# Performance work log

Hardware: AMD Instinct MI355X
Metric: run time of the kernel (lower is better)

Reference implementation:

```python
import jax, jax.numpy as jnp
import numpy as np

B, DM, NH, NL, NP = 4, 768, 12, 3, 4
HD = DM // NH
H_IMG, W_IMG = 896, 896
LEVELS = [(H_IMG // 8, W_IMG // 8), (H_IMG // 16, W_IMG // 16), (H_IMG // 32, W_IMG // 32)]
QH, QW = H_IMG // 14, W_IMG // 14
LQ = QH * QW            # 4096 query tokens (stride-14 ViT grid)
LIN = sum(h * w for h, w in LEVELS)  # 16464 multi-scale value tokens


def setup_inputs() -> dict:
    key = jax.random.key(0)
    ks = jax.random.split(key, 14)
    s = 0.02
    return {
        "query": jax.random.normal(ks[0], (B, LQ, DM), jnp.float32),
        "feat": jax.random.normal(ks[1], (B, LIN, DM), jnp.float32),
        "ln_q_g": jnp.ones((DM,), jnp.float32),
        "ln_q_b": jnp.zeros((DM,), jnp.float32),
        "ln_f_g": jnp.ones((DM,), jnp.float32),
        "ln_f_b": jnp.zeros((DM,), jnp.float32),
        "W_off": jax.random.normal(ks[2], (DM, NH * NL * NP * 2), jnp.float32) * s,
        "b_off": jax.random.normal(ks[3], (NH * NL * NP * 2,), jnp.float32) * s,
        "W_attn": jax.random.normal(ks[4], (DM, NH * NL * NP), jnp.float32) * s,
        "b_attn": jax.random.normal(ks[5], (NH * NL * NP,), jnp.float32) * s,
        "W_val": jax.random.normal(ks[6], (DM, DM), jnp.float32) * s,
        "b_val": jnp.zeros((DM,), jnp.float32),
        "W_out": jax.random.normal(ks[7], (DM, DM), jnp.float32) * s,
        "b_out": jnp.zeros((DM,), jnp.float32),
        "gamma": jax.random.normal(ks[8], (DM,), jnp.float32) * s,
    }


def _ln(x, g, b, eps=1e-6):
    m = x.mean(-1, keepdims=True)
    v = ((x - m) ** 2).mean(-1, keepdims=True)
    return (x - m) * jax.lax.rsqrt(v + eps) * g + b


def _ref_points():
    # get_reference_points for the stride-14 query grid; pixel-center coords normalized
    ry, rx = jnp.meshgrid(
        (jnp.arange(QH, dtype=jnp.float32) + 0.5) / QH,
        (jnp.arange(QW, dtype=jnp.float32) + 0.5) / QW,
        indexing="ij",
    )
    return jnp.stack([rx.reshape(-1), ry.reshape(-1)], -1)  # (LQ, 2) in (x, y)


def _sample_level(v, loc, h_, w_):
    # v: (B, h_, w_, NH, HD); loc: (B, LQ, NH, NP, 2) normalized [0,1]
    # torch grid_sample bilinear, align_corners=False, zero padding
    x = loc[..., 0] * w_ - 0.5
    y = loc[..., 1] * h_ - 0.5
    x0 = jnp.floor(x)
    y0 = jnp.floor(y)
    wx = (x - x0)[..., None]
    wy = (y - y0)[..., None]
    x0i = x0.astype(jnp.int32)
    y0i = y0.astype(jnp.int32)
    bi = jnp.arange(B)[:, None, None, None]
    hi = jnp.arange(NH)[None, None, :, None]

    def g(yi, xi):
        valid = ((xi >= 0) & (xi < w_) & (yi >= 0) & (yi < h_)).astype(v.dtype)
        got = v[bi, jnp.clip(yi, 0, h_ - 1), jnp.clip(xi, 0, w_ - 1), hi]  # (B,LQ,NH,NP,HD)
        return got * valid[..., None]

    v00 = g(y0i, x0i)
    v01 = g(y0i, x0i + 1)
    v10 = g(y0i + 1, x0i)
    v11 = g(y0i + 1, x0i + 1)
    return v00 * (1 - wx) * (1 - wy) + v01 * wx * (1 - wy) + v10 * (1 - wx) * wy + v11 * wx * wy


def _injector(query, feat, ln_q_g, ln_q_b, ln_f_g, ln_f_b, W_off, b_off, W_attn, b_attn,
              W_val, b_val, W_out, b_out, gamma):
    q = _ln(query, ln_q_g, ln_q_b)
    f = _ln(feat, ln_f_g, ln_f_b)
    value = (f @ W_val + b_val).reshape(B, LIN, NH, HD)
    off = (q @ W_off + b_off).reshape(B, LQ, NH, NL, NP, 2)
    aw = jax.nn.softmax((q @ W_attn + b_attn).reshape(B, LQ, NH, NL * NP), axis=-1)
    aw = aw.reshape(B, LQ, NH, NL, NP)
    ref = _ref_points()  # (LQ, 2)
    offset_norm = jnp.array([[w, h] for h, w in LEVELS], jnp.float32)  # (NL, 2) = (W_, H_)
    loc = ref[None, :, None, None, None, :] + off / offset_norm[None, None, None, :, None, :]
    outs = []
    start = 0
    for lvl, (h_, w_) in enumerate(LEVELS):
        v = value[:, start:start + h_ * w_].reshape(B, h_, w_, NH, HD)
        outs.append(_sample_level(v, loc[:, :, :, lvl], h_, w_))
        start += h_ * w_
    samp = jnp.stack(outs, axis=3)  # (B, LQ, NH, NL, NP, HD)
    attn_out = (samp * aw[..., None]).sum(axis=(3, 4)).reshape(B, LQ, DM)
    attn_out = attn_out @ W_out + b_out
    return query + gamma * attn_out


def reference(query, feat, ln_q_g, ln_q_b, ln_f_g, ln_f_b, W_off, b_off, W_attn, b_attn,
              W_val, b_val, W_out, b_out, gamma):
    return _injector(query, feat, ln_q_g, ln_q_b, ln_f_g, ln_f_b, W_off, b_off, W_attn,
                     b_attn, W_val, b_val, W_out, b_out, gamma)
```

## Files before the change

### kernel.cpp

```cpp
#include <hip/hip_runtime.h>
#include <hip/hip_bf16.h>

typedef __hip_bfloat16 bf16;

#define BB    4
#define LQ    4096
#define LIN   16464
#define DM    768
#define NH    12
#define HD    64
#define K_DIM 768

typedef __attribute__((ext_vector_type(8))) __bf16 bfrag;
typedef __attribute__((ext_vector_type(4))) float  ffrag;

__device__ __forceinline__ void g2l16(const void* g, void* l) {
    __builtin_amdgcn_global_load_lds(
        (const __attribute__((address_space(1))) void*)g,
        (__attribute__((address_space(3))) void*)l, 16, 0, 0);
}

__device__ __forceinline__ int xcd_swz(int orig, int nwg) {
    int xcd = orig & 7, within = orig >> 3;
    int q = nwg >> 3, r = nwg & 7;
    return (xcd < r ? xcd * (q + 1) : r * (q + 1) + (xcd - r) * q) + within;
}

__global__ __launch_bounds__(256) void ln_kernel(
    const float* __restrict__ x, const float* __restrict__ g,
    const float* __restrict__ beta, bf16* __restrict__ y)
{
    int r = blockIdx.x * 4 + (threadIdx.x >> 6);
    int lane = threadIdx.x & 63;
    const float4* xr = (const float4*)(x + (size_t)r * DM);
    float4 v[3];
    #pragma unroll
    for (int i = 0; i < 3; i++) v[i] = xr[lane + 64 * i];
    float s = 0.f, ss = 0.f;
    #pragma unroll
    for (int i = 0; i < 3; i++) {
        s  += v[i].x + v[i].y + v[i].z + v[i].w;
        ss += v[i].x * v[i].x + v[i].y * v[i].y + v[i].z * v[i].z + v[i].w * v[i].w;
    }
    #pragma unroll
    for (int m = 1; m <= 32; m <<= 1) {
        s  += __shfl_xor(s, m);
        ss += __shfl_xor(ss, m);
    }
    float mean = s * (1.f / DM);
    float inv  = rsqrtf(ss * (1.f / DM) - mean * mean + 1e-6f);
    bf16* yr = y + (size_t)r * DM;
    #pragma unroll
    for (int i = 0; i < 3; i++) {
        float4 gg = ((const float4*)g)[lane + 64 * i];
        float4 bb = ((const float4*)beta)[lane + 64 * i];
        union { bf16 h[4]; uint2 u; } p;
        p.h[0] = __float2bfloat16((v[i].x - mean) * inv * gg.x + bb.x);
        p.h[1] = __float2bfloat16((v[i].y - mean) * inv * gg.y + bb.y);
        p.h[2] = __float2bfloat16((v[i].z - mean) * inv * gg.z + bb.z);
        p.h[3] = __float2bfloat16((v[i].w - mean) * inv * gg.w + bb.w);
        *(uint2*)(yr + (lane + 64 * i) * 4) = p.u;
    }
}

__global__ __launch_bounds__(256) void cast_transpose(
    const float* __restrict__ W, bf16* __restrict__ Wt, int N)
{
    __shared__ float t[32][33];
    int n0 = blockIdx.x * 32, k0 = blockIdx.y * 32;
    int tx = threadIdx.x & 31, ty = threadIdx.x >> 5;
    #pragma unroll
    for (int i = 0; i < 4; i++) {
        int k = k0 + ty + i * 8;
        int n = n0 + tx;
        t[ty + i * 8][tx] = (n < N) ? W[(size_t)k * N + n] : 0.f;
    }
    __syncthreads();
    #pragma unroll
    for (int i = 0; i < 4; i++) {
        int n = n0 + ty + i * 8;
        Wt[(size_t)n * K_DIM + k0 + tx] = __float2bfloat16(t[tx][ty + i * 8]);
    }
}

__global__ __launch_bounds__(512) void gemm256_value(
    const bf16*  __restrict__ A,
    const bf16*  __restrict__ Bt,
    const float* __restrict__ bias,
    bf16*        __restrict__ C,
    int M, int N)
{
    __shared__ __align__(16) char lds[98304];

    int tid  = threadIdx.x;
    int lane = tid & 63;
    int wave = tid >> 6;

    int nwg  = gridDim.x * gridDim.y;
    int orig = blockIdx.y * gridDim.x + blockIdx.x;
    int wg   = xcd_swz(orig, nwg);
    int bn = (wg % gridDim.x) * 256;
    int bm = (wg / gridDim.x) * 256;

    int ahalf = wave >> 2;
    int wc    = (wave & 3) * 64;

    int mrow = lane & 15;
    int kqs  = (((lane >> 4) ^ ((mrow >> 1) & 3)) * 8);

    ffrag acc[8][4] = {};

    int rA = tid >> 2;
    int kb = (((tid & 3) ^ ((rA >> 1) & 3)) * 8);
    int ra0 = min(bm + rA, M - 1), ra1 = min(bm + 128 + rA, M - 1);
    const bf16* gA0 = A  + (size_t)ra0 * K_DIM + kb;
    const bf16* gA1 = A  + (size_t)ra1 * K_DIM + kb;
    const bf16* gB0 = Bt + (size_t)(bn + rA) * K_DIM + kb;
    const bf16* gB1 = Bt + (size_t)(bn + 128 + rA) * K_DIM + kb;

    auto stage = [&](char* buf, int kt) {
        const int ko = kt * 32;
        g2l16(gA0 + ko, buf + tid * 16);
        g2l16(gA1 + ko, buf + tid * 16 + 8192);
        g2l16(gB0 + ko, buf + 16384 + tid * 16);
        g2l16(gB1 + ko, buf + 16384 + tid * 16 + 8192);
    };

    char* b0 = lds;
    char* b1 = lds + 32768;
    char* b2 = lds + 65536;
    stage(b0, 0); stage(b1, 1); stage(b2, 2);

    #pragma unroll
    for (int kt = 0; kt < 24; kt++) {
        if (kt + 2 < 24)      asm volatile("s_waitcnt vmcnt(8)" ::: "memory");
        else if (kt + 1 < 24) asm volatile("s_waitcnt vmcnt(4)" ::: "memory");
        else                  asm volatile("s_waitcnt vmcnt(0)" ::: "memory");
        __builtin_amdgcn_s_barrier();

        const char* Ab = b0 + (ahalf * 128) * 64;
        const char* Bb = b0 + 16384 + wc * 64;
        bfrag af[8], bf[4];
        #pragma unroll
        for (int mr = 0; mr < 8; mr++)
            af[mr] = *(const bfrag*)(Ab + (mr * 16 + mrow) * 64 + kqs * 2);
        #pragma unroll
        for (int nc = 0; nc < 4; nc++)
            bf[nc] = *(const bfrag*)(Bb + (nc * 16 + mrow) * 64 + kqs * 2);

        __builtin_amdgcn_s_setprio(1);
        #pragma unroll
        for (int mr = 0; mr < 8; mr++)
            #pragma unroll
            for (int nc = 0; nc < 4; nc++)
                acc[mr][nc] = __builtin_amdgcn_mfma_f32_16x16x32_bf16(
                    af[mr], bf[nc], acc[mr][nc], 0, 0, 0);
        __builtin_amdgcn_s_setprio(0);

        __builtin_amdgcn_s_barrier();
        if (kt + 3 < 24) stage(b0, kt + 3);
        char* tp = b0; b0 = b1; b1 = b2; b2 = tp;
    }

    int q4 = (lane >> 4) * 4;
    #pragma unroll
    for (int mr = 0; mr < 8; mr++) {
        #pragma unroll
        for (int rr = 0; rr < 4; rr++) {
            int rg = bm + ahalf * 128 + mr * 16 + q4 + rr;
            if (rg < M) {
                #pragma unroll
                for (int nc = 0; nc < 4; nc++) {
                    int cg = bn + wc + nc * 16 + mrow;
                    C[(size_t)rg * N + cg] =
                        __float2bfloat16(acc[mr][nc][rr] + bias[cg]);
                }
            }
        }
    }
}

__device__ __forceinline__ void gemm128_body(
    const bf16*  __restrict__ A,
    const bf16*  __restrict__ Bt,
    const float* __restrict__ bias,
    void*        __restrict__ C,
    const float* __restrict__ resid,
    const float* __restrict__ gamma,
    const float* __restrict__ bias2,
    int M, int N, int mode, int nsplit, char* lds)
{
    int tid  = threadIdx.x;
    int lane = tid & 63;

    int nwg  = gridDim.x * gridDim.y;
    int orig = blockIdx.y * gridDim.x + blockIdx.x;
    int wg = xcd_swz(orig, nwg);
    int bn = (wg % gridDim.x) * 128;
    int bm = (wg / gridDim.x) * 128;

    int wave = tid >> 6;
    int wr = (wave & 1) * 64, wc = (wave >> 1) * 64;

    ffrag acc[4][4] = {};

    int rA = tid >> 2;
    int kb = (((tid & 3) ^ ((rA >> 1) & 3)) * 8);
    int ra0 = min(bm + rA, M - 1), ra1 = min(bm + 64 + rA, M - 1);
    const bf16* gA0 = A  + (size_t)ra0 * K_DIM + kb;
    const bf16* gA1 = A  + (size_t)ra1 * K_DIM + kb;
    const bf16* gB0 = Bt + (size_t)(bn + rA) * K_DIM + kb;
    const bf16* gB1 = Bt + (size_t)(bn + 64 + rA) * K_DIM + kb;

    int mrow = lane & 15;
    int kqs  = (((lane >> 4) ^ ((mrow >> 1) & 3)) * 8);

    auto stage = [&](char* buf, int kt) {
        const int ko = kt * 32;
        g2l16(gA0 + ko, buf + tid * 16);
        g2l16(gA1 + ko, buf + tid * 16 + 4096);
        g2l16(gB0 + ko, buf + 8192 + tid * 16);
        g2l16(gB1 + ko, buf + 8192 + tid * 16 + 4096);
    };

    stage(lds, 0);
    asm volatile("s_waitcnt vmcnt(0)" ::: "memory");
    __builtin_amdgcn_s_barrier();

    #pragma unroll
    for (int kt = 0; kt < 24; kt++) {
        char* cur = lds + (kt & 1) * 16384;
        char* nxt = lds + ((kt & 1) ^ 1) * 16384;
        if (kt + 1 < 24) stage(nxt, kt + 1);

        bfrag a[4], b[4];
        #pragma unroll
        for (int t = 0; t < 4; t++) {
            a[t] = *(const bfrag*)(cur + ((wr + t * 16 + mrow) * 32 + kqs) * 2);
            b[t] = *(const bfrag*)(cur + 8192 + ((wc + t * 16 + mrow) * 32 + kqs) * 2);
        }
        __builtin_amdgcn_s_setprio(1);
        #pragma unroll
        for (int i = 0; i < 4; i++)
            #pragma unroll
            for (int j = 0; j < 4; j++)
                acc[i][j] = __builtin_amdgcn_mfma_f32_16x16x32_bf16(
                    a[i], b[j], acc[i][j], 0, 0, 0);
        __builtin_amdgcn_s_setprio(0);

        asm volatile("s_waitcnt vmcnt(0)" ::: "memory");
        __builtin_amdgcn_s_barrier();
    }

    int q4 = (lane >> 4) * 4;
    #pragma unroll
    for (int i = 0; i < 4; i++) {
        #pragma unroll
        for (int rr = 0; rr < 4; rr++) {
            int rg = bm + wr + i * 16 + q4 + rr;
            if (rg < M) {
                #pragma unroll
                for (int j = 0; j < 4; j++) {
                    int cg = bn + wc + j * 16 + mrow;
                    if (cg < N) {
                        float bv = (mode == 3 && cg >= nsplit) ? bias2[cg - nsplit]
                                                               : bias[cg];
                        float v = acc[i][j][rr] + bv;
                        size_t idx = (size_t)rg * N + cg;
                        if (mode == 2)      ((float*)C)[idx] = resid[idx] + gamma[cg] * v;
                        else                ((float*)C)[idx] = v;
                    }
                }
            }
        }
    }
}

__global__ __launch_bounds__(256) void gemm128_comb(
    const bf16* __restrict__ A, const bf16* __restrict__ Bt,
    const float* __restrict__ bias, void* __restrict__ C,
    const float* __restrict__ bias2, int M, int N, int nsplit)
{
    __shared__ __align__(16) char lds[32768];
    gemm128_body(A, Bt, bias, C, nullptr, nullptr, bias2, M, N, 3, nsplit, lds);
}

__global__ __launch_bounds__(256) void gemm128_out(
    const bf16* __restrict__ A, const bf16* __restrict__ Bt,
    const float* __restrict__ bias, void* __restrict__ C,
    const float* __restrict__ resid, const float* __restrict__ gamma,
    int M, int N)
{
    __shared__ __align__(16) char lds[32768];
    gemm128_body(A, Bt, bias, C, resid, gamma, nullptr, M, N, 2, 0, lds);
}

__global__ __launch_bounds__(256) void prep_kernel(
    const float* __restrict__ comb, uint4* __restrict__ pre)
{
    int t  = blockIdx.x * 256 + threadIdx.x;
    int p  = t % 12;
    int uh = t / 12;
    int h  = uh % NH;
    int bq = uh / NH;
    int q  = bq & (LQ - 1);
    int b  = bq >> 12;

    const float* rowp = comb + (size_t)bq * 432;
    const float* lg = rowp + 288 + h * 12;

    float4 a4 = ((const float4*)lg)[0];
    float4 b4 = ((const float4*)lg)[1];
    float4 c4 = ((const float4*)lg)[2];
    float mx = fmaxf(fmaxf(fmaxf(fmaxf(a4.x, a4.y), fmaxf(a4.z, a4.w)),
                           fmaxf(fmaxf(b4.x, b4.y), fmaxf(b4.z, b4.w))),
                     fmaxf(fmaxf(c4.x, c4.y), fmaxf(c4.z, c4.w)));
    float den = __expf(a4.x - mx) + __expf(a4.y - mx) + __expf(a4.z - mx) +
                __expf(a4.w - mx) + __expf(b4.x - mx) + __expf(b4.y - mx) +
                __expf(b4.z - mx) + __expf(b4.w - mx) + __expf(c4.x - mx) +
                __expf(c4.y - mx) + __expf(c4.z - mx) + __expf(c4.w - mx);
    float lp  = lg[p];
    float awn = __expf(lp - mx) / den;

    int lvl = p >> 2;
    const int wl = (lvl == 0) ? 112 : (lvl == 1 ? 56 : 28);
    const int sl = (lvl == 0) ? 0   : (lvl == 1 ? 12544 : 15680);

    float2 oxy = *(const float2*)(rowp + h * 24 + p * 2);

    float rx = ((q & 63) + 0.5f) * (1.f / 64.f);
    float ry = ((q >> 6) + 0.5f) * (1.f / 64.f);
    float x = rx * wl + oxy.x - 0.5f;
    float y = ry * wl + oxy.y - 0.5f;
    float xf = floorf(x), yf = floorf(y);
    float wx = x - xf, wy = y - yf;
    int x0 = (int)xf, x1 = x0 + 1;
    int y0 = (int)yf, y1 = y0 + 1;
    bool vx0 = (unsigned)x0 < (unsigned)wl, vx1 = (unsigned)x1 < (unsigned)wl;
    bool vy0 = (unsigned)y0 < (unsigned)wl, vy1 = (unsigned)y1 < (unsigned)wl;
    int x0c = min(max(x0, 0), wl - 1), x1c = min(max(x1, 0), wl - 1);
    int y0c = min(max(y0, 0), wl - 1), y1c = min(max(y1, 0), wl - 1);

    int base = b * LIN + sl;
    int yb0 = (base + y0c * wl) * (NH * HD) + h * HD;
    int yb1 = (base + y1c * wl) * (NH * HD) + h * HD;
    int xb0 = x0c * (NH * HD);
    int xb1 = x1c * (NH * HD);

    float w0x = vx0 ? (1.f - wx) * awn : 0.f;
    float w1x = vx1 ? wx * awn : 0.f;
    float wy0f = vy0 ? (1.f - wy) : 0.f;
    float wy1f = vy1 ? wy : 0.f;

    uint4 i4 = {(unsigned)yb0, (unsigned)yb1, (unsigned)xb0, (unsigned)xb1};
    uint4 w4 = {__float_as_uint(w0x), __float_as_uint(w1x),
                __float_as_uint(wy0f), __float_as_uint(wy1f)};
    pre[(size_t)t * 2 + 0] = i4;
    pre[(size_t)t * 2 + 1] = w4;
}

__global__ __launch_bounds__(256) void sample_kernel(
    const bf16*  __restrict__ value,
    const uint4* __restrict__ pre,
    bf16*        __restrict__ attn)
{
    __shared__ float red[4][8][64];

    int wv   = threadIdx.x >> 6;
    int wg   = xcd_swz(blockIdx.x, gridDim.x);
    int unit = __builtin_amdgcn_readfirstlane((wg << 2) + wv);
    int lane = threadIdx.x & 63;
    int o   = lane & 7;
    int c8  = lane >> 3;
    int k   = c8 & 3;
    bool dx = (k & 1) != 0, dy = (k >> 1) != 0;
    bool hi = (c8 & 4) != 0;
    int h  = unit % NH;
    int bq = unit / NH;

    const uint4* pp = pre + (size_t)unit * 24;
    const bf16*  vbase = value + o * 8;

    float acc[8] = {0.f};

    #pragma unroll
    for (int it = 0; it < 6; it++) {
        const uint4* rec = pp + it * 4 + (hi ? 2 : 0);
        uint4 i4 = rec[0];
        uint4 w4 = rec[1];
        int idx = (dy ? (int)i4.y : (int)i4.x) + (dx ? (int)i4.w : (int)i4.z);
        float w = (dx ? __uint_as_float(w4.y) : __uint_as_float(w4.x)) *
                  (dy ? __uint_as_float(w4.w) : __uint_as_float(w4.z));
        uint4 v = *(const uint4*)(vbase + idx);
        const unsigned* u = (const unsigned*)&v;
        #pragma unroll
        for (int j = 0; j < 4; j++) {
            float f0 = __uint_as_float(u[j] << 16);
            float f1 = __uint_as_float(u[j] & 0xFFFF0000u);
            acc[j * 2 + 0] = fmaf(w, f0, acc[j * 2 + 0]);
            acc[j * 2 + 1] = fmaf(w, f1, acc[j * 2 + 1]);
        }
    }

    {
        float* rw = &red[wv][c8][0];
        int base = (o * 8 + c8 * 4) & 63;
        *(float4*)&rw[base] = float4{acc[0], acc[1], acc[2], acc[3]};
        *(float4*)&rw[(base + 4) & 63] = float4{acc[4], acc[5], acc[6], acc[7]};
    }
    asm volatile("s_waitcnt lgkmcnt(0)" ::: "memory");
    __builtin_amdgcn_sched_barrier(0);
    float sum = 0.f;
    #pragma unroll
    for (int s = 0; s < 8; s++)
        sum += red[wv][s][(lane + s * 4) & 63];

    attn[(size_t)bq * DM + h * HD + lane] = __float2bfloat16(sum);
}

extern "C" void kernel_launch(void* const* d_in, const int* in_sizes, int n_in,
                              void* d_out, int out_size, void* d_ws, size_t ws_size,
                              hipStream_t stream)
{
    const float* query  = (const float*)d_in[0];
    const float* feat   = (const float*)d_in[1];
    const float* ln_q_g = (const float*)d_in[2];
    const float* ln_q_b = (const float*)d_in[3];
    const float* ln_f_g = (const float*)d_in[4];
    const float* ln_f_b = (const float*)d_in[5];
    const float* W_off  = (const float*)d_in[6];
    const float* b_off  = (const float*)d_in[7];
    const float* W_attn = (const float*)d_in[8];
    const float* b_attn = (const float*)d_in[9];
    const float* W_val  = (const float*)d_in[10];
    const float* b_val  = (const float*)d_in[11];
    const float* W_out  = (const float*)d_in[12];
    const float* b_out  = (const float*)d_in[13];
    const float* gamma  = (const float*)d_in[14];
    float* out = (float*)d_out;

    char* ws = (char*)d_ws;
    char* od = (char*)d_out;
    const int M_F = BB * LIN;
    const int M_Q = BB * LQ;

    bf16*  value  = (bf16*)(ws);
    bf16*  f_ln   = (bf16*)(ws + 101154816);
    bf16*  Wt_out = (bf16*)(ws + 101154816);
    uint4* pre    = (uint4*)(ws + 101154816 + 4194304);
    bf16*  q_ln   = (bf16*)(ws + 202309632);
    bf16*  attn   = (bf16*)(ws + 202309632);

    bf16*  Wt_val  = (bf16*)(od);
    bf16*  Wt_comb = (bf16*)(od + 1179648);
    float* comb    = (float*)(od + 2162688);

    cast_transpose<<<dim3(24, 24), 256, 0, stream>>>(W_val, Wt_val, 768);
    cast_transpose<<<dim3(9, 24), 256, 0, stream>>>(W_off, Wt_comb, 288);
    cast_transpose<<<dim3(7, 24), 256, 0, stream>>>(
        W_attn, Wt_comb + (size_t)288 * K_DIM, 144);

    ln_kernel<<<M_F / 4, 256, 0, stream>>>(feat, ln_f_g, ln_f_b, f_ln);
    ln_kernel<<<M_Q / 4, 256, 0, stream>>>(query, ln_q_g, ln_q_b, q_ln);

    gemm256_value<<<dim3(3, (M_F + 255) / 256), 512, 0, stream>>>(
        f_ln, Wt_val, b_val, value, M_F, DM);

    cast_transpose<<<dim3(24, 24), 256, 0, stream>>>(W_out, Wt_out, 768);

    gemm128_comb<<<dim3(4, M_Q / 128), 256, 0, stream>>>(
        q_ln, Wt_comb, b_off, comb, b_attn, M_Q, 432, 288);

    prep_kernel<<<(M_Q * NH * 12) / 256, 256, 0, stream>>>(comb, pre);

    sample_kernel<<<(M_Q * NH) / 4, 256, 0, stream>>>(value, pre, attn);

    gemm128_out<<<dim3(6, M_Q / 128), 256, 0, stream>>>(
        attn, Wt_out, b_out, out, query, gamma, M_Q, DM);
}
```

Before: 708.4 us.

## Precompute per-corner index/weight pairs and batch gathers; double-buffer value GEMM

The precompute kernel now stores four (index, weight) pairs, one per bilinear corner, instead of separate y/x offsets and weight factors. Each sample lane therefore loads one 8-byte record with no select or multiply. The sample kernel issues all six record loads and then all six value gathers before accumulating, which puts more memory requests in flight. Separately, the value GEMM drops from triple to double LDS buffering (64KB instead of 96KB), which could raise occupancy but shortens the prefetch distance.

```diff
diff --git a/kernel.cpp b/kernel.cpp
--- a/kernel.cpp
+++ b/kernel.cpp
@@ -90,7 +90,7 @@
     bf16*        __restrict__ C,
     int M, int N)
 {
-    __shared__ __align__(16) char lds[98304];
+    __shared__ __align__(16) char lds[65536];
 
     int tid  = threadIdx.x;
     int lane = tid & 63;
@@ -128,14 +128,12 @@
 
     char* b0 = lds;
     char* b1 = lds + 32768;
-    char* b2 = lds + 65536;
-    stage(b0, 0); stage(b1, 1); stage(b2, 2);
+    stage(b0, 0); stage(b1, 1);
 
     #pragma unroll
     for (int kt = 0; kt < 24; kt++) {
-        if (kt + 2 < 24)      asm volatile("s_waitcnt vmcnt(8)" ::: "memory");
-        else if (kt + 1 < 24) asm volatile("s_waitcnt vmcnt(4)" ::: "memory");
-        else                  asm volatile("s_waitcnt vmcnt(0)" ::: "memory");
+        if (kt + 1 < 24) asm volatile("s_waitcnt vmcnt(4)" ::: "memory");
+        else             asm volatile("s_waitcnt vmcnt(0)" ::: "memory");
         __builtin_amdgcn_s_barrier();
 
         const char* Ab = b0 + (ahalf * 128) * 64;
@@ -158,8 +156,8 @@
         __builtin_amdgcn_s_setprio(0);
 
         __builtin_amdgcn_s_barrier();
-        if (kt + 3 < 24) stage(b0, kt + 3);
-        char* tp = b0; b0 = b1; b1 = b2; b2 = tp;
+        if (kt + 2 < 24) stage(b0, kt + 2);
+        char* tp = b0; b0 = b1; b1 = tp;
     }
 
     int q4 = (lane >> 4) * 4;
@@ -347,16 +345,17 @@
     int xb0 = x0c * (NH * HD);
     int xb1 = x1c * (NH * HD);
 
-    float w0x = vx0 ? (1.f - wx) * awn : 0.f;
-    float w1x = vx1 ? wx * awn : 0.f;
+    float wx0 = vx0 ? (1.f - wx) * awn : 0.f;
+    float wx1 = vx1 ? wx * awn : 0.f;
     float wy0f = vy0 ? (1.f - wy) : 0.f;
     float wy1f = vy1 ? wy : 0.f;
 
-    uint4 i4 = {(unsigned)yb0, (unsigned)yb1, (unsigned)xb0, (unsigned)xb1};
-    uint4 w4 = {__float_as_uint(w0x), __float_as_uint(w1x),
-                __float_as_uint(wy0f), __float_as_uint(wy1f)};
-    pre[(size_t)t * 2 + 0] = i4;
-    pre[(size_t)t * 2 + 1] = w4;
+    uint4 r0 = {(unsigned)(yb0 + xb0), __float_as_uint(wx0 * wy0f),
+                (unsigned)(yb0 + xb1), __float_as_uint(wx1 * wy0f)};
+    uint4 r1 = {(unsigned)(yb1 + xb0), __float_as_uint(wx0 * wy1f),
+                (unsigned)(yb1 + xb1), __float_as_uint(wx1 * wy1f)};
+    pre[(size_t)t * 2 + 0] = r0;
+    pre[(size_t)t * 2 + 1] = r1;
 }
 
 __global__ __launch_bounds__(256) void sample_kernel(
@@ -373,26 +372,28 @@
     int o   = lane & 7;
     int c8  = lane >> 3;
     int k   = c8 & 3;
-    bool dx = (k & 1) != 0, dy = (k >> 1) != 0;
-    bool hi = (c8 & 4) != 0;
+    int hi  = (c8 >> 2) & 1;
     int h  = unit % NH;
     int bq = unit / NH;
 
-    const uint4* pp = pre + (size_t)unit * 24;
-    const bf16*  vbase = value + o * 8;
+    const uint2* pr = (const uint2*)((const char*)pre
+        + (size_t)unit * 384 + hi * 32 + k * 8);
+
+    uint2 rec[6];
+    #pragma unroll
+    for (int it = 0; it < 6; it++) rec[it] = pr[it * 8];
+
+    const bf16* vb = value + o * 8;
+    uint4 v[6];
+    #pragma unroll
+    for (int it = 0; it < 6; it++)
+        v[it] = *(const uint4*)(vb + (int)rec[it].x);
 
     float acc[8] = {0.f};
-
     #pragma unroll
     for (int it = 0; it < 6; it++) {
-        const uint4* rec = pp + it * 4 + (hi ? 2 : 0);
-        uint4 i4 = rec[0];
-        uint4 w4 = rec[1];
-        int idx = (dy ? (int)i4.y : (int)i4.x) + (dx ? (int)i4.w : (int)i4.z);
-        float w = (dx ? __uint_as_float(w4.y) : __uint_as_float(w4.x)) *
-                  (dy ? __uint_as_float(w4.w) : __uint_as_float(w4.z));
-        uint4 v = *(const uint4*)(vbase + idx);
-        const unsigned* u = (const unsigned*)&v;
+        float w = __uint_as_float(rec[it].y);
+        const unsigned* u = (const unsigned*)&v[it];
         #pragma unroll
         for (int j = 0; j < 4; j++) {
             float f0 = __uint_as_float(u[j] << 16);
```

Measured after the change: 669.8 us. 1.06x faster.
